# Optimization experiments

Hardware: AMD Instinct MI355X
Metric: run time of the kernel (lower is better)

Reference implementation:

```python
import jax, jax.numpy as jnp
import numpy as np

C = 128                      # channels per irrep
LS = [0, 0, 1, 1, 2, 2]      # active irreps (0e,0o,1e,1o,2e,2o), sorted order
D = C * sum(2 * l + 1 for l in LS)  # 2304
N = 100000                   # nodes


def setup_inputs() -> dict:
    key = jax.random.key(0)
    ks = jax.random.split(key, 7)
    inp = {"x": jax.random.normal(ks[0], (N, D), dtype=jnp.float32)}
    scale = 1.0 / np.sqrt(C)
    for name, k in zip(["W0p", "W0m", "W1p", "W1m", "W2p", "W2m"], ks[1:]):
        inp[name] = jax.random.normal(k, (C, C), dtype=jnp.float32) * scale
    return inp


def reference(x, W0p, W0m, W1p, W1m, W2p, W2m):
    # Split flat features into per-(l,parity) blocks [N, C, 2l+1],
    # mix channels per irrep (movedim + Linear in torch == einsum here),
    # merge back and add residual.
    Ws = [W0p, W0m, W1p, W1m, W2p, W2m]
    idx = 0
    parts = []
    for l, W in zip(LS, Ws):
        d = C * (2 * l + 1)
        blk = x[:, idx:idx + d].reshape(-1, C, 2 * l + 1)  # [N, C, m]
        idx += d
        y = jnp.einsum('ncm,dc->ndm', blk, W)              # channel mix per m
        parts.append(y.reshape(-1, d))
    return x + jnp.concatenate(parts, axis=-1)
```

## Files before the change

### kernel.cpp

```cpp
#include <hip/hip_runtime.h>

typedef float f32x4 __attribute__((ext_vector_type(4)));
typedef short s16x8 __attribute__((ext_vector_type(8)));

__device__ __forceinline__ unsigned short f32_to_bf16(float f){
    union { float f; unsigned u; } v; v.f = f;
    unsigned r = v.u + 0x7fffu + ((v.u >> 16) & 1u);
    return (unsigned short)(r >> 16);
}
__device__ __forceinline__ unsigned pack2(float a, float b){
    return (unsigned)f32_to_bf16(a) | ((unsigned)f32_to_bf16(b) << 16);
}

__global__ __launch_bounds__(256)
void wconv_kernel(const float* __restrict__ W0p, const float* __restrict__ W0m,
                  const float* __restrict__ W1p, const float* __restrict__ W1m,
                  const float* __restrict__ W2p, const float* __restrict__ W2m,
                  unsigned short* __restrict__ wbf)
{
    const int idx = blockIdx.x * 256 + threadIdx.x;
    const int w  = idx >> 14;
    const int rc = idx & 16383;
    const float* Wp;
    switch (w) {
        case 0: Wp = W0p; break;  case 1: Wp = W0m; break;
        case 2: Wp = W1p; break;  case 3: Wp = W1m; break;
        case 4: Wp = W2p; break;  default: Wp = W2m; break;
    }
    const float v = Wp[rc] + (((rc >> 7) == (rc & 127)) ? 1.0f : 0.0f);
    wbf[idx] = f32_to_bf16(v);
}

__global__ __launch_bounds__(256)
void l0_kernel(const float* __restrict__ x, const unsigned short* __restrict__ wbf,
               float* __restrict__ out)
{
    constexpr int LDSS = 264;
    __shared__ __attribute__((aligned(16))) unsigned short lin[16 * LDSS];

    const size_t nbase = (size_t)blockIdx.x * 16;
    const int tid = threadIdx.x;
    const int wv  = tid >> 6, ln = tid & 63;
    const int l16 = ln & 15,  lhi = ln >> 4;

    const float* src = x + nbase * 2304;
    #pragma unroll
    for (int i = 0; i < 4; ++i) {
        const int f  = i * 1024 + tid * 4;
        const int nl = f >> 8, c = f & 255;
        const float4 v = *reinterpret_cast<const float4*>(src + (size_t)nl * 2304 + c);
        uint2 p; p.x = pack2(v.x, v.y); p.y = pack2(v.z, v.w);
        *reinterpret_cast<uint2*>(&lin[nl * LDSS + c]) = p;
    }
    __syncthreads();

    const int b     = wv >> 1;
    const int dbase = (wv & 1) * 64;
    const unsigned short* wb = wbf + b * 16384;

    f32x4 acc[4];
    #pragma unroll
    for (int dt = 0; dt < 4; ++dt) acc[dt] = (f32x4){0.f,0.f,0.f,0.f};

    #pragma unroll
    for (int s = 0; s < 4; ++s) {
        const int k0 = s * 32 + lhi * 8;
        const s16x8 bf = *reinterpret_cast<const s16x8*>(&lin[l16 * LDSS + b * 128 + k0]);
        #pragma unroll
        for (int dt = 0; dt < 4; ++dt) {
            const int d = dbase + dt * 16 + l16;
            const s16x8 af = *reinterpret_cast<const s16x8*>(wb + d * 128 + k0);
            acc[dt] = __builtin_amdgcn_mfma_f32_16x16x32_bf16(af, bf, acc[dt], 0, 0, 0);
        }
    }

    float* dst = out + (nbase + l16) * 2304 + b * 128 + dbase + lhi * 4;
    #pragma unroll
    for (int dt = 0; dt < 4; ++dt) {
        float4 v; v.x = acc[dt][0]; v.y = acc[dt][1]; v.z = acc[dt][2]; v.w = acc[dt][3];
        *reinterpret_cast<float4*>(dst + dt * 16) = v;
    }
}

template<int ML, int NT>
__global__ __launch_bounds__(256)
void lx_kernel(const float* __restrict__ x, const unsigned short* __restrict__ wbf,
               float* __restrict__ out, int yoff0, int yoff1, int w0)
{
    constexpr int BLK  = 128 * ML;
    constexpr int ROWS = NT * ML;
    constexpr int RT   = ROWS / 16;
    constexpr int LDSS = 136;
    constexpr int QPT  = (NT * 32) / 256;
    constexpr int ITER = NT * BLK / 1024;
    constexpr int H    = (RT + 1) / 2;

    constexpr size_t IN_B  = (size_t)ROWS * LDSS * 2;
    constexpr size_t OUT_B = (size_t)NT * BLK * 4;
    constexpr size_t SMEM  = OUT_B > IN_B ? OUT_B : IN_B;
    __shared__ __attribute__((aligned(16))) char smem[SMEM];
    unsigned short* lin  = (unsigned short*)smem;
    float*          lout = (float*)smem;

    const int yoff = blockIdx.y ? yoff1 : yoff0;
    const unsigned short* wb = wbf + (size_t)(w0 + blockIdx.y) * 16384;
    const size_t nbase = (size_t)blockIdx.x * NT;

    const int tid = threadIdx.x;
    const int wv  = tid >> 6, ln = tid & 63;
    const int l16 = ln & 15,  lhi = ln >> 4;

    const float* src = x + nbase * 2304 + yoff;
    #pragma unroll
    for (int i = 0; i < QPT; ++i) {
        const int q  = i * 256 + tid;
        const int nl = q >> 5;
        const int c  = (q & 31) * 4;
        const float* p = src + (size_t)nl * 2304 + c * ML;
        float v[4 * ML];
        #pragma unroll
        for (int j = 0; j < ML; ++j) {
            const float4 t = *reinterpret_cast<const float4*>(p + j * 4);
            v[j*4+0] = t.x; v[j*4+1] = t.y; v[j*4+2] = t.z; v[j*4+3] = t.w;
        }
        #pragma unroll
        for (int mm = 0; mm < ML; ++mm) {
            uint2 pk;
            pk.x = pack2(v[mm], v[mm + ML]);
            pk.y = pack2(v[mm + 2*ML], v[mm + 3*ML]);
            const int row = nl * ML + mm;
            *reinterpret_cast<uint2*>(&lin[row * LDSS + c]) = pk;
        }
    }
    __syncthreads();

    const int th = wv >> 1, ch = wv & 1;
    const int t0 = th * H;

    f32x4 acc[H][4];
    #pragma unroll
    for (int rt = 0; rt < H; ++rt)
        #pragma unroll
        for (int tf = 0; tf < 4; ++tf) acc[rt][tf] = (f32x4){0.f,0.f,0.f,0.f};

    #pragma unroll
    for (int s = 0; s < 4; ++s) {
        const int k0 = s * 32 + lhi * 8;
        s16x8 bf[4];
        #pragma unroll
        for (int tf = 0; tf < 4; ++tf) {
            const int d = ch * 64 + tf * 16 + l16;
            bf[tf] = *reinterpret_cast<const s16x8*>(wb + d * 128 + k0);
        }
        #pragma unroll
        for (int rt = 0; rt < H; ++rt) {
            if (t0 + rt < RT) {
                const int row = (t0 + rt) * 16 + l16;
                const s16x8 af = *reinterpret_cast<const s16x8*>(&lin[row * LDSS + k0]);
                #pragma unroll
                for (int tf = 0; tf < 4; ++tf)
                    acc[rt][tf] = __builtin_amdgcn_mfma_f32_16x16x32_bf16(af, bf[tf], acc[rt][tf], 0, 0, 0);
            }
        }
    }
    __syncthreads();

    #pragma unroll
    for (int rt = 0; rt < H; ++rt) {
        if (t0 + rt < RT) {
            #pragma unroll
            for (int tf = 0; tf < 4; ++tf) {
                const int col = ch * 64 + tf * 16 + l16;
                #pragma unroll
                for (int j = 0; j < 4; ++j) {
                    const int row = (t0 + rt) * 16 + lhi * 4 + j;
                    const int nl  = row / ML;
                    const int mm  = row - nl * ML;
                    lout[nl * BLK + col * ML + mm] = acc[rt][tf][j];
                }
            }
        }
    }
    __syncthreads();

    float* dst = out + nbase * 2304 + yoff;
    #pragma unroll
    for (int i = 0; i < ITER; ++i) {
        const int f  = (i * 256 + tid) * 4;
        const int nl = f / BLK;
        const int r  = f - nl * BLK;
        *reinterpret_cast<float4*>(dst + (size_t)nl * 2304 + r) =
            *reinterpret_cast<const float4*>(&lout[f]);
    }
}

extern "C" void kernel_launch(void* const* d_in, const int* in_sizes, int n_in,
                              void* d_out, int out_size, void* d_ws, size_t ws_size,
                              hipStream_t stream) {
    const float* x   = (const float*)d_in[0];
    const float* W0p = (const float*)d_in[1];
    const float* W0m = (const float*)d_in[2];
    const float* W1p = (const float*)d_in[3];
    const float* W1m = (const float*)d_in[4];
    const float* W2p = (const float*)d_in[5];
    const float* W2m = (const float*)d_in[6];
    float* out = (float*)d_out;
    unsigned short* wbf = (unsigned short*)d_ws;

    const int N = in_sizes[0] / 2304;

    wconv_kernel<<<384, 256, 0, stream>>>(W0p, W0m, W1p, W1m, W2p, W2m, wbf);

    lx_kernel<5,16><<<dim3(N/16, 2), 256, 0, stream>>>(x, wbf, out, 1024, 1664, 4);
    lx_kernel<3,32><<<dim3(N/32, 2), 256, 0, stream>>>(x, wbf, out, 256,  640,  2);
    l0_kernel      <<<N/16,          256, 0, stream>>>(x, wbf, out);
}
```

Before: 464.2 us.

## Fuse per-irrep GEMM kernels into one interleaved-bucket kernel with smaller tiles

Replaces the three separate per-l launches with a single fused kernel. Each group of 13 blocks covers a 32-node bucket: 8 blocks do l=2 (8 nodes each), 4 do l=1 (16 nodes each) and 1 does l=0 (32 nodes). This removes the launch gaps and tail effects between kernels and mixes work types so a row of x is read by blocks that are close in time. It also shrinks tile sizes, which permits partial 16-row MFMA tiles (l=2 gives 40 rows) and needs an extra bounds check. The bf16 packing now uses the HIP intrinsic, and the grid size is hardcoded for N=100000.

```diff
diff --git a/kernel.cpp b/kernel.cpp
--- a/kernel.cpp
+++ b/kernel.cpp
@@ -1,7 +1,10 @@
 #include <hip/hip_runtime.h>
+#include <hip/hip_bf16.h>
 
 typedef float f32x4 __attribute__((ext_vector_type(4)));
 typedef short s16x8 __attribute__((ext_vector_type(8)));
+
+#define SMEM_BYTES 24576
 
 __device__ __forceinline__ unsigned short f32_to_bf16(float f){
     union { float f; unsigned u; } v; v.f = f;
@@ -9,7 +12,10 @@
     return (unsigned short)(r >> 16);
 }
 __device__ __forceinline__ unsigned pack2(float a, float b){
-    return (unsigned)f32_to_bf16(a) | ((unsigned)f32_to_bf16(b) << 16);
+    float2 t; t.x = a; t.y = b;
+    __hip_bfloat162 h = __float22bfloat162_rn(t);
+    union { __hip_bfloat162 h; unsigned u; } c; c.h = h;
+    return c.u;
 }
 
 __global__ __launch_bounds__(256)
@@ -31,92 +37,34 @@
     wbf[idx] = f32_to_bf16(v);
 }
 
-__global__ __launch_bounds__(256)
-void l0_kernel(const float* __restrict__ x, const unsigned short* __restrict__ wbf,
-               float* __restrict__ out)
-{
-    constexpr int LDSS = 264;
-    __shared__ __attribute__((aligned(16))) unsigned short lin[16 * LDSS];
-
-    const size_t nbase = (size_t)blockIdx.x * 16;
+template<int ML, int NT>
+__device__ __forceinline__
+void lx_body(const float* __restrict__ src0, const unsigned short* __restrict__ wb,
+             float* __restrict__ dst0, int tile, char* smem)
+{
+    constexpr int BLK   = 128 * ML;
+    constexpr int RROWS = NT * ML;
+    constexpr int RTC   = (RROWS + 15) / 16;
+    constexpr int H     = (RTC + 1) / 2;
+    constexpr int LDSS  = 136;
+    constexpr int QPT   = NT * 32 / 256;
+    constexpr int ITER  = NT * BLK / 1024;
+
+    unsigned short* lin  = (unsigned short*)smem;
+    float*          lout = (float*)smem;
+
+    const size_t nbase = (size_t)tile * NT;
     const int tid = threadIdx.x;
     const int wv  = tid >> 6, ln = tid & 63;
     const int l16 = ln & 15,  lhi = ln >> 4;
 
-    const float* src = x + nbase * 2304;
-    #pragma unroll
-    for (int i = 0; i < 4; ++i) {
-        const int f  = i * 1024 + tid * 4;
-        const int nl = f >> 8, c = f & 255;
-        const float4 v = *reinterpret_cast<const float4*>(src + (size_t)nl * 2304 + c);
-        uint2 p; p.x = pack2(v.x, v.y); p.y = pack2(v.z, v.w);
-        *reinterpret_cast<uint2*>(&lin[nl * LDSS + c]) = p;
-    }
-    __syncthreads();
-
-    const int b     = wv >> 1;
-    const int dbase = (wv & 1) * 64;
-    const unsigned short* wb = wbf + b * 16384;
-
-    f32x4 acc[4];
-    #pragma unroll
-    for (int dt = 0; dt < 4; ++dt) acc[dt] = (f32x4){0.f,0.f,0.f,0.f};
-
-    #pragma unroll
-    for (int s = 0; s < 4; ++s) {
-        const int k0 = s * 32 + lhi * 8;
-        const s16x8 bf = *reinterpret_cast<const s16x8*>(&lin[l16 * LDSS + b * 128 + k0]);
-        #pragma unroll
-        for (int dt = 0; dt < 4; ++dt) {
-            const int d = dbase + dt * 16 + l16;
-            const s16x8 af = *reinterpret_cast<const s16x8*>(wb + d * 128 + k0);
-            acc[dt] = __builtin_amdgcn_mfma_f32_16x16x32_bf16(af, bf, acc[dt], 0, 0, 0);
-        }
-    }
-
-    float* dst = out + (nbase + l16) * 2304 + b * 128 + dbase + lhi * 4;
-    #pragma unroll
-    for (int dt = 0; dt < 4; ++dt) {
-        float4 v; v.x = acc[dt][0]; v.y = acc[dt][1]; v.z = acc[dt][2]; v.w = acc[dt][3];
-        *reinterpret_cast<float4*>(dst + dt * 16) = v;
-    }
-}
-
-template<int ML, int NT>
-__global__ __launch_bounds__(256)
-void lx_kernel(const float* __restrict__ x, const unsigned short* __restrict__ wbf,
-               float* __restrict__ out, int yoff0, int yoff1, int w0)
-{
-    constexpr int BLK  = 128 * ML;
-    constexpr int ROWS = NT * ML;
-    constexpr int RT   = ROWS / 16;
-    constexpr int LDSS = 136;
-    constexpr int QPT  = (NT * 32) / 256;
-    constexpr int ITER = NT * BLK / 1024;
-    constexpr int H    = (RT + 1) / 2;
-
-    constexpr size_t IN_B  = (size_t)ROWS * LDSS * 2;
-    constexpr size_t OUT_B = (size_t)NT * BLK * 4;
-    constexpr size_t SMEM  = OUT_B > IN_B ? OUT_B : IN_B;
-    __shared__ __attribute__((aligned(16))) char smem[SMEM];
-    unsigned short* lin  = (unsigned short*)smem;
-    float*          lout = (float*)smem;
-
-    const int yoff = blockIdx.y ? yoff1 : yoff0;
-    const unsigned short* wb = wbf + (size_t)(w0 + blockIdx.y) * 16384;
-    const size_t nbase = (size_t)blockIdx.x * NT;
-
-    const int tid = threadIdx.x;
-    const int wv  = tid >> 6, ln = tid & 63;
-    const int l16 = ln & 15,  lhi = ln >> 4;
-
-    const float* src = x + nbase * 2304 + yoff;
+    const float* src = src0 + nbase * 2304;
     #pragma unroll
     for (int i = 0; i < QPT; ++i) {
         const int q  = i * 256 + tid;
         const int nl = q >> 5;
-        const int c  = (q & 31) * 4;
-        const float* p = src + (size_t)nl * 2304 + c * ML;
+        const int c4 = (q & 31) * 4;
+        const float* p = src + (size_t)nl * 2304 + c4 * ML;
         float v[4 * ML];
         #pragma unroll
         for (int j = 0; j < ML; ++j) {
@@ -128,8 +76,7 @@
             uint2 pk;
             pk.x = pack2(v[mm], v[mm + ML]);
             pk.y = pack2(v[mm + 2*ML], v[mm + 3*ML]);
-            const int row = nl * ML + mm;
-            *reinterpret_cast<uint2*>(&lin[row * LDSS + c]) = pk;
+            *reinterpret_cast<uint2*>(&lin[(nl * ML + mm) * LDSS + c4]) = pk;
         }
     }
     __syncthreads();
@@ -148,15 +95,13 @@
         const int k0 = s * 32 + lhi * 8;
         s16x8 bf[4];
         #pragma unroll
-        for (int tf = 0; tf < 4; ++tf) {
-            const int d = ch * 64 + tf * 16 + l16;
-            bf[tf] = *reinterpret_cast<const s16x8*>(wb + d * 128 + k0);
-        }
+        for (int tf = 0; tf < 4; ++tf)
+            bf[tf] = *reinterpret_cast<const s16x8*>(wb + (ch * 64 + tf * 16 + l16) * 128 + k0);
         #pragma unroll
         for (int rt = 0; rt < H; ++rt) {
-            if (t0 + rt < RT) {
-                const int row = (t0 + rt) * 16 + l16;
-                const s16x8 af = *reinterpret_cast<const s16x8*>(&lin[row * LDSS + k0]);
+            if (t0 + rt < RTC) {
+                const s16x8 af = *reinterpret_cast<const s16x8*>(
+                    &lin[((t0 + rt) * 16 + l16) * LDSS + k0]);
                 #pragma unroll
                 for (int tf = 0; tf < 4; ++tf)
                     acc[rt][tf] = __builtin_amdgcn_mfma_f32_16x16x32_bf16(af, bf[tf], acc[rt][tf], 0, 0, 0);
@@ -167,30 +112,119 @@
 
     #pragma unroll
     for (int rt = 0; rt < H; ++rt) {
-        if (t0 + rt < RT) {
+        if (t0 + rt < RTC) {
             #pragma unroll
             for (int tf = 0; tf < 4; ++tf) {
                 const int col = ch * 64 + tf * 16 + l16;
                 #pragma unroll
                 for (int j = 0; j < 4; ++j) {
                     const int row = (t0 + rt) * 16 + lhi * 4 + j;
-                    const int nl  = row / ML;
-                    const int mm  = row - nl * ML;
-                    lout[nl * BLK + col * ML + mm] = acc[rt][tf][j];
+                    if (row < RROWS) {
+                        const int nl = row / ML;
+                        const int mm = row - nl * ML;
+                        lout[nl * BLK + col * ML + mm] = acc[rt][tf][j];
+                    }
                 }
             }
         }
     }
     __syncthreads();
 
-    float* dst = out + nbase * 2304 + yoff;
+    float* dst = dst0 + nbase * 2304;
     #pragma unroll
     for (int i = 0; i < ITER; ++i) {
         const int f  = (i * 256 + tid) * 4;
         const int nl = f / BLK;
-        const int r  = f - nl * BLK;
-        *reinterpret_cast<float4*>(dst + (size_t)nl * 2304 + r) =
+        const int rr = f - nl * BLK;
+        *reinterpret_cast<float4*>(dst + (size_t)nl * 2304 + rr) =
             *reinterpret_cast<const float4*>(&lout[f]);
+    }
+}
+
+__device__ __forceinline__
+void l0_body(const float* __restrict__ x, const unsigned short* __restrict__ wbf,
+             float* __restrict__ out, int tile, char* smem)
+{
+    constexpr int LDSS = 264;
+    unsigned short* lin = (unsigned short*)smem;
+
+    const size_t nbase = (size_t)tile * 32;
+    const int tid = threadIdx.x;
+    const int wv  = tid >> 6, ln = tid & 63;
+    const int l16 = ln & 15,  lhi = ln >> 4;
+
+    const float* src = x + nbase * 2304;
+    #pragma unroll
+    for (int i = 0; i < 8; ++i) {
+        const int f  = i * 1024 + tid * 4;
+        const int nl = f >> 8, c = f & 255;
+        const float4 v = *reinterpret_cast<const float4*>(src + (size_t)nl * 2304 + c);
+        uint2 p; p.x = pack2(v.x, v.y); p.y = pack2(v.z, v.w);
+        *reinterpret_cast<uint2*>(&lin[nl * LDSS + c]) = p;
+    }
+    __syncthreads();
+
+    const int b     = wv >> 1;
+    const int dbase = (wv & 1) * 64;
+    const unsigned short* wb = wbf + b * 16384;
+
+    f32x4 acc[2][4];
+    #pragma unroll
+    for (int nt = 0; nt < 2; ++nt)
+        #pragma unroll
+        for (int dt = 0; dt < 4; ++dt) acc[nt][dt] = (f32x4){0.f,0.f,0.f,0.f};
+
+    #pragma unroll
+    for (int s = 0; s < 4; ++s) {
+        const int k0 = s * 32 + lhi * 8;
+        s16x8 af[4];
+        #pragma unroll
+        for (int dt = 0; dt < 4; ++dt)
+            af[dt] = *reinterpret_cast<const s16x8*>(wb + (dbase + dt * 16 + l16) * 128 + k0);
+        #pragma unroll
+        for (int nt = 0; nt < 2; ++nt) {
+            const s16x8 bfv = *reinterpret_cast<const s16x8*>(
+                &lin[(nt * 16 + l16) * LDSS + b * 128 + k0]);
+            #pragma unroll
+            for (int dt = 0; dt < 4; ++dt)
+                acc[nt][dt] = __builtin_amdgcn_mfma_f32_16x16x32_bf16(af[dt], bfv, acc[nt][dt], 0, 0, 0);
+        }
+    }
+
+    #pragma unroll
+    for (int nt = 0; nt < 2; ++nt) {
+        float* dst = out + (nbase + nt * 16 + l16) * 2304 + b * 128 + dbase + lhi * 4;
+        #pragma unroll
+        for (int dt = 0; dt < 4; ++dt) {
+            float4 v; v.x = acc[nt][dt][0]; v.y = acc[nt][dt][1];
+                      v.z = acc[nt][dt][2]; v.w = acc[nt][dt][3];
+            *reinterpret_cast<float4*>(dst + dt * 16) = v;
+        }
+    }
+}
+
+__global__ __launch_bounds__(256)
+void fused_kernel(const float* __restrict__ x, const unsigned short* __restrict__ wbf,
+                  float* __restrict__ out)
+{
+    __shared__ __attribute__((aligned(16))) char smem[SMEM_BYTES];
+    const int bucket = blockIdx.x / 13;
+    const int r      = blockIdx.x - bucket * 13;
+
+    if (r < 8) {
+        const int idx    = bucket * 8 + r;
+        const int parity = idx & 1;
+        const int tile   = idx >> 1;
+        const int off    = parity ? 1664 : 1024;
+        lx_body<5, 8>(x + off, wbf + (size_t)(4 + parity) * 16384, out + off, tile, smem);
+    } else if (r < 12) {
+        const int idx    = bucket * 4 + (r - 8);
+        const int parity = idx & 1;
+        const int tile   = idx >> 1;
+        const int off    = parity ? 640 : 256;
+        lx_body<3, 16>(x + off, wbf + (size_t)(2 + parity) * 16384, out + off, tile, smem);
+    } else {
+        l0_body(x, wbf, out, bucket, smem);
     }
 }
 
@@ -207,11 +241,6 @@
     float* out = (float*)d_out;
     unsigned short* wbf = (unsigned short*)d_ws;
 
-    const int N = in_sizes[0] / 2304;
-
     wconv_kernel<<<384, 256, 0, stream>>>(W0p, W0m, W1p, W1m, W2p, W2m, wbf);
-
-    lx_kernel<5,16><<<dim3(N/16, 2), 256, 0, stream>>>(x, wbf, out, 1024, 1664, 4);
-    lx_kernel<3,32><<<dim3(N/32, 2), 256, 0, stream>>>(x, wbf, out, 256,  640,  2);
-    l0_kernel      <<<N/16,          256, 0, stream>>>(x, wbf, out);
-}
+    fused_kernel<<<40625, 256, 0, stream>>>(x, wbf, out);
+}
```

Measured after the change: 478.5 us. 3.1% more time.
